# Kernel optimization log

Measured on AMD Instinct MI355X. Metric: run time of the kernel, lower is better.

## Reference

```python
import jax, jax.numpy as jnp
import numpy as np

N = 100000      # nodes
E = 1600000     # edges
IN = 64; H = 64; OUT = 64
ED = 32         # edge_dim
L = 2           # num_layers
NT = 3          # num_node_types
ET = 4          # num_edge_types
EPS = 1e-5


def setup_inputs() -> dict:
    key = jax.random.key(0)
    ks = jax.random.split(key, 16)
    x = jax.random.normal(ks[0], (N, IN), dtype=jnp.float32)
    edge_index = jax.random.randint(ks[1], (2, E), 0, N, dtype=jnp.int64)
    edge_attr = jax.random.normal(ks[2], (E, ED), dtype=jnp.float32)
    node_type = jax.random.randint(ks[3], (N,), 0, NT, dtype=jnp.int64)
    edge_type = jax.random.randint(ks[4], (E,), 0, ET, dtype=jnp.int64)
    # parameters (stacked over layers; layer0 in_channels == hidden so shapes match)
    Wn = jax.random.normal(ks[5], (L, NT, H, H), dtype=jnp.float32) * 0.05   # per-node-type linear
    bn = jax.random.normal(ks[6], (L, NT, H), dtype=jnp.float32) * 0.05
    Wm = jax.random.normal(ks[7], (L, ET, ED), dtype=jnp.float32) * 0.1     # edge MLP Linear(ED,1)
    bm = jax.random.normal(ks[8], (L, ET), dtype=jnp.float32) * 0.1
    emb = jax.random.normal(ks[9], (L, ET, ED), dtype=jnp.float32) * 0.1    # edge_type_emb
    ln_g = jnp.ones((L, H), dtype=jnp.float32)
    ln_b = jnp.zeros((L, H), dtype=jnp.float32)
    fc_w = jax.random.normal(ks[10], (OUT, H), dtype=jnp.float32) * 0.05
    fc_b = jnp.zeros((OUT,), dtype=jnp.float32)
    return {"x": x, "edge_index": edge_index, "edge_attr": edge_attr,
            "node_type": node_type, "edge_type": edge_type,
            "Wn": Wn, "bn": bn, "Wm": Wm, "bm": bm, "emb": emb,
            "ln_g": ln_g, "ln_b": ln_b, "fc_w": fc_w, "fc_b": fc_b}


def _layernorm(h, g, b):
    mu = jnp.mean(h, axis=-1, keepdims=True)
    var = jnp.mean((h - mu) ** 2, axis=-1, keepdims=True)
    return (h - mu) * jax.lax.rsqrt(var + EPS) * g + b


def reference(x, edge_index, edge_attr, node_type, edge_type,
              Wn, bn, Wm, bm, emb, ln_g, ln_b, fc_w, fc_b):
    src = edge_index[0]  # x_j
    dst = edge_index[1]  # x_i (aggregation target)
    for l in range(L):
        # HydroConv message: softplus(edge MLP per edge type) * (x_j - x_i)
        ea = edge_attr + emb[l][edge_type]                               # [E, ED]
        w = jax.nn.softplus(jnp.einsum('ed,ed->e', ea, Wm[l][edge_type])
                            + bm[l][edge_type])                          # [E]
        msg = w[:, None] * (x[src] - x[dst])                             # [E, H]
        aggr = jax.ops.segment_sum(msg, dst, num_segments=N)            # [N, H]
        # per-node-type linear update
        h = jnp.einsum('nd,ndo->no', aggr, Wn[l][node_type]) + bn[l][node_type]
        h = jax.nn.relu(h)
        x = _layernorm(h, ln_g[l], ln_b[l])
    return x @ fc_w.T + fc_b
```

## Files before the change

kernel.cpp:

```cpp
#include <hip/hip_runtime.h>

#define NN 100000
#define NE 1600000
#define HDIM 64
#define EDIM 32
#define NTT 3
#define ETT 4
#define NTILES 6250
#define LEPS 1e-5f
#define NBKT 782
#define EPB 8192
#define NWGA 196
#define SCAP 4096
#define NSC (NBKT * NWGA)
#define SBLK 150

typedef _Float16 half2v __attribute__((ext_vector_type(2)));
typedef _Float16 half4v __attribute__((ext_vector_type(4)));
typedef _Float16 half8v __attribute__((ext_vector_type(8)));
typedef float f32x4 __attribute__((ext_vector_type(4)));

__global__ void prep_kernel(const float* __restrict__ Wn, const float* __restrict__ fc_w,
                            _Float16* __restrict__ Wp, _Float16* __restrict__ fcp) {
    const int i = blockIdx.x * blockDim.x + threadIdx.x;
    if (i < 6 * HDIM * HDIM) {
        const int lt = i >> 12;
        const int o = (i >> 6) & 63;
        const int d = i & 63;
        Wp[i] = (_Float16)Wn[((size_t)lt * 64 + d) * 64 + o];
    } else if (i < 6 * HDIM * HDIM + HDIM * HDIM) {
        const int j = i - 6 * HDIM * HDIM;
        fcp[j] = (_Float16)fc_w[j];
    }
}

__global__ __launch_bounds__(256) void edge_weights_kernel(
        const float* __restrict__ edge_attr,
        const int* __restrict__ eisrc,
        const int* __restrict__ edge_type,
        const float* __restrict__ Wm,
        const float* __restrict__ bm,
        const float* __restrict__ emb,
        int2* __restrict__ ewu) {
    __shared__ float sWm[2 * ETT * EDIM];
    __shared__ float sc[2 * ETT];
    const int tid = threadIdx.x;
    if (tid < 2 * ETT * EDIM) sWm[tid] = Wm[tid];
    __syncthreads();
    if (tid < 2 * ETT) {
        float c = bm[tid];
        #pragma unroll
        for (int k = 0; k < EDIM; k++) c += emb[tid * EDIM + k] * sWm[tid * EDIM + k];
        sc[tid] = c;
    }
    __syncthreads();
    const int lane = tid & 63;
    const int wv = tid >> 6;
    const int sub = lane >> 3;
    const int k = lane & 7;
    const int ebase = blockIdx.x * 128 + wv * 32;
    #pragma unroll
    for (int it = 0; it < 4; it++) {
        const int e = ebase + it * 8 + sub;
        const int et = edge_type[e];
        const float4 v = ((const float4*)(edge_attr + (size_t)e * EDIM))[k];
        const float4 a = ((const float4*)(sWm + et * EDIM))[k];
        const float4 b = ((const float4*)(sWm + (ETT + et) * EDIM))[k];
        float d0 = v.x * a.x + v.y * a.y + v.z * a.z + v.w * a.w;
        float d1 = v.x * b.x + v.y * b.y + v.z * b.z + v.w * b.w;
        d0 += __shfl_xor(d0, 1); d1 += __shfl_xor(d1, 1);
        d0 += __shfl_xor(d0, 2); d1 += __shfl_xor(d1, 2);
        d0 += __shfl_xor(d0, 4); d1 += __shfl_xor(d1, 4);
        if (k == 0) {
            d0 += sc[et];
            d1 += sc[ETT + et];
            const float w0 = fmaxf(d0, 0.f) + log1pf(expf(-fabsf(d0)));
            const float w1 = fmaxf(d1, 0.f) + log1pf(expf(-fabsf(d1)));
            union { half2v h; int i; } u;
            u.h[0] = (_Float16)w0;
            u.h[1] = (_Float16)w1;
            ewu[e] = make_int2(u.i, eisrc[e]);
        }
    }
}

__global__ void xcvt_kernel(const float* __restrict__ x, _Float16* __restrict__ xs) {
    const int i = blockIdx.x * blockDim.x + threadIdx.x;
    const float4 v = ((const float4*)x)[i];
    half4v o = { (_Float16)v.x, (_Float16)v.y, (_Float16)v.z, (_Float16)v.w };
    ((half4v*)xs)[i] = o;
}

__global__ __launch_bounds__(256) void hist_kernel(const int* __restrict__ eidst,
                                                   int* __restrict__ whist) {
    __shared__ int h[NBKT];
    for (int i = threadIdx.x; i < NBKT; i += 256) h[i] = 0;
    __syncthreads();
    const int wg = blockIdx.x;
    const int start = wg * EPB, end = min(start + EPB, NE);
    for (int e = start + threadIdx.x; e < end; e += 256)
        atomicAdd(&h[eidst[e] >> 7], 1);
    __syncthreads();
    for (int i = threadIdx.x; i < NBKT; i += 256) whist[i * NWGA + wg] = h[i];
}

__global__ __launch_bounds__(256) void partial2_kernel(const int* __restrict__ in,
                                                       int* __restrict__ psum) {
    __shared__ int red[256];
    const int b = blockIdx.x, t = threadIdx.x;
    const int base = b * 1024 + t * 4;
    int s = 0;
    #pragma unroll
    for (int k = 0; k < 4; k++) { const int i = base + k; if (i < NSC) s += in[i]; }
    red[t] = s;
    __syncthreads();
    for (int d = 128; d > 0; d >>= 1) {
        if (t < d) red[t] += red[t + d];
        __syncthreads();
    }
    if (t == 0) psum[b] = red[0];
}

__global__ void bscan2_kernel(const int* __restrict__ psum, int* __restrict__ poff) {
    __shared__ int v[256];
    const int t = threadIdx.x;
    v[t] = (t < SBLK) ? psum[t] : 0;
    __syncthreads();
    for (int d = 1; d < 256; d <<= 1) {
        const int x = (t >= d) ? v[t - d] : 0;
        __syncthreads();
        v[t] += x;
        __syncthreads();
    }
    poff[t] = (t == 0) ? 0 : v[t - 1];
}

__global__ __launch_bounds__(256) void wscan2_kernel(const int* __restrict__ in,
                                                     const int* __restrict__ poff,
                                                     int* __restrict__ out) {
    __shared__ int red[256];
    const int b = blockIdx.x, t = threadIdx.x;
    const int base = b * 1024 + t * 4;
    int d4[4];
    #pragma unroll
    for (int k = 0; k < 4; k++) d4[k] = (base + k < NSC) ? in[base + k] : 0;
    const int s = d4[0] + d4[1] + d4[2] + d4[3];
    red[t] = s;
    __syncthreads();
    for (int d = 1; d < 256; d <<= 1) {
        const int x = (t >= d) ? red[t - d] : 0;
        __syncthreads();
        red[t] += x;
        __syncthreads();
    }
    int run = poff[b] + ((t == 0) ? 0 : red[t - 1]);
    #pragma unroll
    for (int k = 0; k < 4; k++) {
        if (base + k < NSC) { out[base + k] = run; run += d4[k]; }
    }
}

__global__ __launch_bounds__(256) void binb_kernel(const int2* __restrict__ ewu,
                                                   const int* __restrict__ eidst,
                                                   const int* __restrict__ wscan,
                                                   int2* __restrict__ brec) {
    __shared__ int lcur[NBKT];
    const int wg = blockIdx.x;
    for (int i = threadIdx.x; i < NBKT; i += 256) lcur[i] = wscan[i * NWGA + wg];
    __syncthreads();
    const int start = wg * EPB, end = min(start + EPB, NE);
    for (int e = start + threadIdx.x; e < end; e += 256) {
        const int dst = eidst[e];
        const int2 r = ewu[e];
        const int pos = atomicAdd(&lcur[dst >> 7], 1);
        brec[pos] = make_int2(r.x, r.y | ((dst & 127) << 17));
    }
}

__global__ __launch_bounds__(256) void sortb_kernel(const int2* __restrict__ brec,
                                                    const int* __restrict__ wscan,
                                                    int* __restrict__ off,
                                                    int2* __restrict__ ews) {
    __shared__ int hist[128];
    __shared__ int excl[128];
    __shared__ int2 sorted[SCAP];
    const int b = blockIdx.x;
    const int node0 = b << 7;
    const int nn = min(128, NN - node0);
    const int base = wscan[b * NWGA];
    const int end = (b < NBKT - 1) ? wscan[(b + 1) * NWGA] : NE;
    const int n = end - base;
    const int t = threadIdx.x;
    if (t < 128) hist[t] = 0;
    __syncthreads();
    for (int i = t; i < n; i += 256)
        atomicAdd(&hist[(brec[base + i].y >> 17) & 127], 1);
    __syncthreads();
    if (t < 128) excl[t] = hist[t];
    __syncthreads();
    for (int d = 1; d < 128; d <<= 1) {
        int v = 0;
        if (t < 128 && t >= d) v = excl[t - d];
        __syncthreads();
        if (t < 128) excl[t] += v;
        __syncthreads();
    }
    if (t < 128) {
        const int ex = excl[t] - hist[t];
        if (t < nn) off[node0 + t] = base + ex;
        hist[t] = ex;
    }
    if (b == NBKT - 1 && t == 0) off[NN] = NE;
    __syncthreads();
    for (int i = t; i < n; i += 256) {
        const int2 r = brec[base + i];
        const int dstl = (r.y >> 17) & 127;
        const int2 o = make_int2(r.x, r.y & 0x1FFFF);
        const int pos = atomicAdd(&hist[dstl], 1);
        if (pos < SCAP) sorted[pos] = o;
        else ews[base + pos] = o;
    }
    __syncthreads();
    const int m = min(n, SCAP);
    for (int i = t; i < m; i += 256) ews[base + i] = sorted[i];
}

template<int LAYER>
__global__ __launch_bounds__(512) void gather_kernel(const _Float16* __restrict__ xs,
                                                     const int2* __restrict__ ew,
                                                     const int* __restrict__ off,
                                                     _Float16* __restrict__ aggr) {
    const int lane = threadIdx.x & 63;
    const int wid = threadIdx.x >> 6;
    const int p = blockIdx.x * 8 + wid;
    const int g = lane >> 4;
    const int fl = lane & 15;
    const int lo = off[p], hi = off[p + 1];
    float a0 = 0.f, a1 = 0.f, a2 = 0.f, a3 = 0.f, sw = 0.f;
    for (int base = lo; base < hi; base += 4) {
        const int i = base + g;
        if (i < hi) {
            const int2 e = ew[i];
            union { int i; half2v h; } u; u.i = e.x;
            const float w = (float)u.h[LAYER];
            const half4v xv = *(const half4v*)(xs + (size_t)e.y * HDIM + fl * 4);
            a0 += w * (float)xv[0];
            a1 += w * (float)xv[1];
            a2 += w * (float)xv[2];
            a3 += w * (float)xv[3];
            sw += w;
        }
    }
    a0 += __shfl_xor(a0, 16); a1 += __shfl_xor(a1, 16);
    a2 += __shfl_xor(a2, 16); a3 += __shfl_xor(a3, 16);
    sw += __shfl_xor(sw, 16);
    a0 += __shfl_xor(a0, 32); a1 += __shfl_xor(a1, 32);
    a2 += __shfl_xor(a2, 32); a3 += __shfl_xor(a3, 32);
    sw += __shfl_xor(sw, 32);
    const half4v xt = *(const half4v*)(xs + (size_t)p * HDIM + fl * 4);
    a0 -= sw * (float)xt[0];
    a1 -= sw * (float)xt[1];
    a2 -= sw * (float)xt[2];
    a3 -= sw * (float)xt[3];
    if (g == 0) {
        half4v o = { (_Float16)a0, (_Float16)a1, (_Float16)a2, (_Float16)a3 };
        *(half4v*)(aggr + (size_t)p * HDIM + fl * 4) = o;
    }
}

template<int FUSE>
__global__ __launch_bounds__(256) void update_kernel(const _Float16* __restrict__ aggr,
                                                     const int* __restrict__ ntype,
                                                     const _Float16* __restrict__ Wp,
                                                     const float* __restrict__ bnp,
                                                     const float* __restrict__ lng,
                                                     const float* __restrict__ lnb,
                                                     const _Float16* __restrict__ fcp,
                                                     const float* __restrict__ fcb,
                                                     _Float16* __restrict__ xout,
                                                     float* __restrict__ fout) {
    __shared__ float scst[320];
    __shared__ f32x4 sraw[4 * 4608 / 16];
    for (int i = threadIdx.x; i < 320; i += 256)
        scst[i] = (i < 192) ? bnp[i] : ((i < 256) ? lng[i - 192] : lnb[i - 256]);
    __syncthreads();

    const int wid = threadIdx.x >> 6;
    const int lane = threadIdx.x & 63;
    const int tile = blockIdx.x * 4 + wid;
    if (tile >= NTILES) return;
    const int fl = lane & 15;
    const int gq = lane >> 4;
    const size_t R = (size_t)tile * 16;

    const half8v A0 = *(const half8v*)(aggr + (R + fl) * HDIM + gq * 8);
    const half8v A1 = *(const half8v*)(aggr + (R + fl) * HDIM + 32 + gq * 8);
    int nt[4];
    #pragma unroll
    for (int r = 0; r < 4; r++) nt[r] = ntype[R + gq * 4 + r];

    float h[4][4];
    #pragma unroll
    for (int ob = 0; ob < 4; ob++) {
        const int col = ob * 16 + fl;
        f32x4 c[3];
        #pragma unroll
        for (int t = 0; t < 3; t++) {
            const half8v B0 = *(const half8v*)(Wp + t * 4096 + col * 64 + gq * 8);
            const half8v B1 = *(const half8v*)(Wp + t * 4096 + col * 64 + 32 + gq * 8);
            f32x4 z = { 0.f, 0.f, 0.f, 0.f };
            z = __builtin_amdgcn_mfma_f32_16x16x32_f16(A0, B0, z, 0, 0, 0);
            z = __builtin_amdgcn_mfma_f32_16x16x32_f16(A1, B1, z, 0, 0, 0);
            c[t] = z;
        }
        #pragma unroll
        for (int r = 0; r < 4; r++) {
            float v = (nt[r] == 0) ? c[0][r] : ((nt[r] == 1) ? c[1][r] : c[2][r]);
            v += scst[nt[r] * 64 + col];
            h[ob][r] = fmaxf(v, 0.f);
        }
    }

    float mu[4], rs[4];
    #pragma unroll
    for (int r = 0; r < 4; r++) {
        float m = h[0][r] + h[1][r] + h[2][r] + h[3][r];
        m += __shfl_xor(m, 1); m += __shfl_xor(m, 2);
        m += __shfl_xor(m, 4); m += __shfl_xor(m, 8);
        mu[r] = m * (1.f / 64.f);
        const float d0 = h[0][r] - mu[r], d1 = h[1][r] - mu[r];
        const float d2 = h[2][r] - mu[r], d3 = h[3][r] - mu[r];
        float v = d0 * d0 + d1 * d1 + d2 * d2 + d3 * d3;
        v += __shfl_xor(v, 1); v += __shfl_xor(v, 2);
        v += __shfl_xor(v, 4); v += __shfl_xor(v, 8);
        rs[r] = rsqrtf(v * (1.f / 64.f) + LEPS);
    }

    _Float16* wb = (_Float16*)sraw + (size_t)wid * 2304;
    #pragma unroll
    for (int ob = 0; ob < 4; ob++) {
        const int col = ob * 16 + fl;
        const float gg = scst[192 + col], bb = scst[256 + col];
        #pragma unroll
        for (int r = 0; r < 4; r++) {
            const float xn = (h[ob][r] - mu[r]) * rs[r] * gg + bb;
            wb[(gq * 4 + r) * 72 + col] = (_Float16)xn;
        }
    }
    __threadfence_block();

    if (!FUSE) {
        const int rr = lane >> 2, cg = lane & 3;
        const half8v o0 = *(const half8v*)(wb + rr * 72 + cg * 16);
        const half8v o1 = *(const half8v*)(wb + rr * 72 + cg * 16 + 8);
        *(half8v*)(xout + (R + rr) * HDIM + cg * 16) = o0;
        *(half8v*)(xout + (R + rr) * HDIM + cg * 16 + 8) = o1;
    } else {
        const half8v FA0 = *(const half8v*)(wb + fl * 72 + gq * 8);
        const half8v FA1 = *(const half8v*)(wb + fl * 72 + 32 + gq * 8);
        float fo[4][4];
        #pragma unroll
        for (int ob = 0; ob < 4; ob++) {
            const int col = ob * 16 + fl;
            const half8v FB0 = *(const half8v*)(fcp + col * 64 + gq * 8);
            const half8v FB1 = *(const half8v*)(fcp + col * 64 + 32 + gq * 8);
            f32x4 z = { 0.f, 0.f, 0.f, 0.f };
            z = __builtin_amdgcn_mfma_f32_16x16x32_f16(FA0, FB0, z, 0, 0, 0);
            z = __builtin_amdgcn_mfma_f32_16x16x32_f16(FA1, FB1, z, 0, 0, 0);
            const float fb = fcb[col];
            #pragma unroll
            for (int r = 0; r < 4; r++) fo[ob][r] = z[r] + fb;
        }
        __threadfence_block();
        float* fb32 = (float*)((char*)sraw + (size_t)wid * 4608);
        #pragma unroll
        for (int ob = 0; ob < 4; ob++) {
            const int col = ob * 16 + fl;
            #pragma unroll
            for (int r = 0; r < 4; r++) fb32[(gq * 4 + r) * 68 + col] = fo[ob][r];
        }
        __threadfence_block();
        #pragma unroll
        for (int rr = 0; rr < 16; rr++)
            fout[(R + rr) * HDIM + lane] = fb32[rr * 68 + lane];
    }
}

extern "C" void kernel_launch(void* const* d_in, const int* in_sizes, int n_in,
                              void* d_out, int out_size, void* d_ws, size_t ws_size,
                              hipStream_t stream) {
    const float* x         = (const float*)d_in[0];
    const int*   ei        = (const int*)d_in[1];
    const float* edge_attr = (const float*)d_in[2];
    const int*   node_type = (const int*)d_in[3];
    const int*   edge_type = (const int*)d_in[4];
    const float* Wn        = (const float*)d_in[5];
    const float* bn        = (const float*)d_in[6];
    const float* Wm        = (const float*)d_in[7];
    const float* bm        = (const float*)d_in[8];
    const float* emb       = (const float*)d_in[9];
    const float* ln_g      = (const float*)d_in[10];
    const float* ln_b      = (const float*)d_in[11];
    const float* fc_w      = (const float*)d_in[12];
    const float* fc_b      = (const float*)d_in[13];
    float* out = (float*)d_out;

    char* W = (char*)d_ws;
    int2*      ewu  = (int2*)W;
    int2*      ews  = (int2*)(W + 12800000);
    _Float16*  xs   = (_Float16*)(W + 25600000);
    _Float16*  x1s  = (_Float16*)(W + 38400000);
    _Float16*  aggr = (_Float16*)(W + 51200000);
    int2*      brec = (int2*)(W + 64000000);
    char*      p3   = W + 76800000;
    _Float16*  Wp   = (_Float16*)p3;
    _Float16*  fcp  = (_Float16*)(p3 + 49152);
    int*       off  = (int*)(p3 + 49152 + 8192);
    int*       psum2 = off + NN + 16;
    int*       poff2 = psum2 + 256;
    int*       whist = poff2 + 256;
    int*       wscan = whist + NSC;

    prep_kernel<<<112, 256, 0, stream>>>(Wn, fc_w, Wp, fcp);
    edge_weights_kernel<<<NE / 128, 256, 0, stream>>>(edge_attr, ei, edge_type,
                                                      Wm, bm, emb, ewu);
    xcvt_kernel<<<6250, 256, 0, stream>>>(x, xs);

    hist_kernel<<<NWGA, 256, 0, stream>>>(ei + NE, whist);
    partial2_kernel<<<SBLK, 256, 0, stream>>>(whist, psum2);
    bscan2_kernel<<<1, 256, 0, stream>>>(psum2, poff2);
    wscan2_kernel<<<SBLK, 256, 0, stream>>>(whist, poff2, wscan);
    binb_kernel<<<NWGA, 256, 0, stream>>>(ewu, ei + NE, wscan, brec);
    sortb_kernel<<<NBKT, 256, 0, stream>>>(brec, wscan, off, ews);

    gather_kernel<0><<<NN / 8, 512, 0, stream>>>(xs, ews, off, aggr);
    update_kernel<0><<<(NTILES + 3) / 4, 256, 0, stream>>>(aggr, node_type,
        Wp, bn, ln_g, ln_b, fcp, fc_b, x1s, nullptr);
    gather_kernel<1><<<NN / 8, 512, 0, stream>>>(x1s, ews, off, aggr);
    update_kernel<1><<<(NTILES + 3) / 4, 256, 0, stream>>>(aggr, node_type,
        Wp + 3 * 4096, bn + NTT * HDIM, ln_g + HDIM, ln_b + HDIM, fcp, fc_b, nullptr, out);
}
```

Measured before the change: 332.8 us.

## Fuse gather and per-type update into one layer kernel via shared memory

```diff
diff --git a/kernel.cpp b/kernel.cpp
--- a/kernel.cpp
+++ b/kernel.cpp
@@ -225,76 +225,83 @@
     for (int i = t; i < m; i += 256) ews[base + i] = sorted[i];
 }
 
-template<int LAYER>
-__global__ __launch_bounds__(512) void gather_kernel(const _Float16* __restrict__ xs,
-                                                     const int2* __restrict__ ew,
-                                                     const int* __restrict__ off,
-                                                     _Float16* __restrict__ aggr) {
-    const int lane = threadIdx.x & 63;
-    const int wid = threadIdx.x >> 6;
-    const int p = blockIdx.x * 8 + wid;
-    const int g = lane >> 4;
-    const int fl = lane & 15;
-    const int lo = off[p], hi = off[p + 1];
-    float a0 = 0.f, a1 = 0.f, a2 = 0.f, a3 = 0.f, sw = 0.f;
-    for (int base = lo; base < hi; base += 4) {
-        const int i = base + g;
-        if (i < hi) {
-            const int2 e = ew[i];
-            union { int i; half2v h; } u; u.i = e.x;
-            const float w = (float)u.h[LAYER];
-            const half4v xv = *(const half4v*)(xs + (size_t)e.y * HDIM + fl * 4);
-            a0 += w * (float)xv[0];
-            a1 += w * (float)xv[1];
-            a2 += w * (float)xv[2];
-            a3 += w * (float)xv[3];
-            sw += w;
-        }
-    }
-    a0 += __shfl_xor(a0, 16); a1 += __shfl_xor(a1, 16);
-    a2 += __shfl_xor(a2, 16); a3 += __shfl_xor(a3, 16);
-    sw += __shfl_xor(sw, 16);
-    a0 += __shfl_xor(a0, 32); a1 += __shfl_xor(a1, 32);
-    a2 += __shfl_xor(a2, 32); a3 += __shfl_xor(a3, 32);
-    sw += __shfl_xor(sw, 32);
-    const half4v xt = *(const half4v*)(xs + (size_t)p * HDIM + fl * 4);
-    a0 -= sw * (float)xt[0];
-    a1 -= sw * (float)xt[1];
-    a2 -= sw * (float)xt[2];
-    a3 -= sw * (float)xt[3];
-    if (g == 0) {
-        half4v o = { (_Float16)a0, (_Float16)a1, (_Float16)a2, (_Float16)a3 };
-        *(half4v*)(aggr + (size_t)p * HDIM + fl * 4) = o;
-    }
-}
-
-template<int FUSE>
-__global__ __launch_bounds__(256) void update_kernel(const _Float16* __restrict__ aggr,
-                                                     const int* __restrict__ ntype,
-                                                     const _Float16* __restrict__ Wp,
-                                                     const float* __restrict__ bnp,
-                                                     const float* __restrict__ lng,
-                                                     const float* __restrict__ lnb,
-                                                     const _Float16* __restrict__ fcp,
-                                                     const float* __restrict__ fcb,
-                                                     _Float16* __restrict__ xout,
-                                                     float* __restrict__ fout) {
+template<int LAYER, int FUSE>
+__global__ __launch_bounds__(512) void layer_kernel(
+        const _Float16* __restrict__ xs,
+        const int2* __restrict__ ew,
+        const int* __restrict__ off,
+        const int* __restrict__ ntype,
+        const _Float16* __restrict__ Wp,
+        const float* __restrict__ bnp,
+        const float* __restrict__ lng,
+        const float* __restrict__ lnb,
+        const _Float16* __restrict__ fcp,
+        const float* __restrict__ fcb,
+        _Float16* __restrict__ xout,
+        float* __restrict__ fout) {
     __shared__ float scst[320];
-    __shared__ f32x4 sraw[4 * 4608 / 16];
-    for (int i = threadIdx.x; i < 320; i += 256)
+    __shared__ _Float16 wb[16 * 72];
+    __shared__ float fb32[16 * 68];
+    const int tid = threadIdx.x;
+    for (int i = tid; i < 320; i += 512)
         scst[i] = (i < 192) ? bnp[i] : ((i < 256) ? lng[i - 192] : lnb[i - 256]);
-    __syncthreads();
-
-    const int wid = threadIdx.x >> 6;
-    const int lane = threadIdx.x & 63;
-    const int tile = blockIdx.x * 4 + wid;
-    if (tile >= NTILES) return;
+
+    const int wv = tid >> 6;
+    const int lane = tid & 63;
+    const int sub = lane >> 3;
+    const int k = lane & 7;
+    const size_t R = (size_t)blockIdx.x * 16;
+
+    #pragma unroll
+    for (int rep = 0; rep < 2; rep++) {
+        const int nl = wv * 2 + rep;
+        const int p = (int)R + nl;
+        const int lo = off[p], hi = off[p + 1];
+        float a0 = 0.f, a1 = 0.f, a2 = 0.f, a3 = 0.f;
+        float a4 = 0.f, a5 = 0.f, a6 = 0.f, a7 = 0.f, sw = 0.f;
+        for (int base = lo; base < hi; base += 8) {
+            const int i = base + sub;
+            if (i < hi) {
+                const int2 e = ew[i];
+                union { int i; half2v h; } u; u.i = e.x;
+                const float w = (float)u.h[LAYER];
+                const half8v xv = *(const half8v*)(xs + (size_t)e.y * HDIM + k * 8);
+                a0 += w * (float)xv[0]; a1 += w * (float)xv[1];
+                a2 += w * (float)xv[2]; a3 += w * (float)xv[3];
+                a4 += w * (float)xv[4]; a5 += w * (float)xv[5];
+                a6 += w * (float)xv[6]; a7 += w * (float)xv[7];
+                sw += w;
+            }
+        }
+        #pragma unroll
+        for (int d = 8; d < 64; d <<= 1) {
+            a0 += __shfl_xor(a0, d); a1 += __shfl_xor(a1, d);
+            a2 += __shfl_xor(a2, d); a3 += __shfl_xor(a3, d);
+            a4 += __shfl_xor(a4, d); a5 += __shfl_xor(a5, d);
+            a6 += __shfl_xor(a6, d); a7 += __shfl_xor(a7, d);
+            sw += __shfl_xor(sw, d);
+        }
+        if (sub == 0) {
+            const half8v xt = *(const half8v*)(xs + (size_t)((int)R + nl) * HDIM + k * 8);
+            half8v o;
+            o[0] = (_Float16)(a0 - sw * (float)xt[0]);
+            o[1] = (_Float16)(a1 - sw * (float)xt[1]);
+            o[2] = (_Float16)(a2 - sw * (float)xt[2]);
+            o[3] = (_Float16)(a3 - sw * (float)xt[3]);
+            o[4] = (_Float16)(a4 - sw * (float)xt[4]);
+            o[5] = (_Float16)(a5 - sw * (float)xt[5]);
+            o[6] = (_Float16)(a6 - sw * (float)xt[6]);
+            o[7] = (_Float16)(a7 - sw * (float)xt[7]);
+            *(half8v*)(&wb[nl * 72 + k * 8]) = o;
+        }
+    }
+    __syncthreads();
+    if (wv != 0) return;
+
     const int fl = lane & 15;
     const int gq = lane >> 4;
-    const size_t R = (size_t)tile * 16;
-
-    const half8v A0 = *(const half8v*)(aggr + (R + fl) * HDIM + gq * 8);
-    const half8v A1 = *(const half8v*)(aggr + (R + fl) * HDIM + 32 + gq * 8);
+    const half8v A0 = *(const half8v*)(&wb[fl * 72 + gq * 8]);
+    const half8v A1 = *(const half8v*)(&wb[fl * 72 + 32 + gq * 8]);
     int nt[4];
     #pragma unroll
     for (int r = 0; r < 4; r++) nt[r] = ntype[R + gq * 4 + r];
@@ -336,7 +343,6 @@
         rs[r] = rsqrtf(v * (1.f / 64.f) + LEPS);
     }
 
-    _Float16* wb = (_Float16*)sraw + (size_t)wid * 2304;
     #pragma unroll
     for (int ob = 0; ob < 4; ob++) {
         const int col = ob * 16 + fl;
@@ -351,13 +357,13 @@
 
     if (!FUSE) {
         const int rr = lane >> 2, cg = lane & 3;
-        const half8v o0 = *(const half8v*)(wb + rr * 72 + cg * 16);
-        const half8v o1 = *(const half8v*)(wb + rr * 72 + cg * 16 + 8);
+        const half8v o0 = *(const half8v*)(&wb[rr * 72 + cg * 16]);
+        const half8v o1 = *(const half8v*)(&wb[rr * 72 + cg * 16 + 8]);
         *(half8v*)(xout + (R + rr) * HDIM + cg * 16) = o0;
         *(half8v*)(xout + (R + rr) * HDIM + cg * 16 + 8) = o1;
     } else {
-        const half8v FA0 = *(const half8v*)(wb + fl * 72 + gq * 8);
-        const half8v FA1 = *(const half8v*)(wb + fl * 72 + 32 + gq * 8);
+        const half8v FA0 = *(const half8v*)(&wb[fl * 72 + gq * 8]);
+        const half8v FA1 = *(const half8v*)(&wb[fl * 72 + 32 + gq * 8]);
         float fo[4][4];
         #pragma unroll
         for (int ob = 0; ob < 4; ob++) {
@@ -371,8 +377,6 @@
             #pragma unroll
             for (int r = 0; r < 4; r++) fo[ob][r] = z[r] + fb;
         }
-        __threadfence_block();
-        float* fb32 = (float*)((char*)sraw + (size_t)wid * 4608);
         #pragma unroll
         for (int ob = 0; ob < 4; ob++) {
             const int col = ob * 16 + fl;
@@ -410,9 +414,8 @@
     int2*      ews  = (int2*)(W + 12800000);
     _Float16*  xs   = (_Float16*)(W + 25600000);
     _Float16*  x1s  = (_Float16*)(W + 38400000);
-    _Float16*  aggr = (_Float16*)(W + 51200000);
-    int2*      brec = (int2*)(W + 64000000);
-    char*      p3   = W + 76800000;
+    int2*      brec = (int2*)(W + 51200000);
+    char*      p3   = W + 64000000;
     _Float16*  Wp   = (_Float16*)p3;
     _Float16*  fcp  = (_Float16*)(p3 + 49152);
     int*       off  = (int*)(p3 + 49152 + 8192);
@@ -433,10 +436,9 @@
     binb_kernel<<<NWGA, 256, 0, stream>>>(ewu, ei + NE, wscan, brec);
     sortb_kernel<<<NBKT, 256, 0, stream>>>(brec, wscan, off, ews);
 
-    gather_kernel<0><<<NN / 8, 512, 0, stream>>>(xs, ews, off, aggr);
-    update_kernel<0><<<(NTILES + 3) / 4, 256, 0, stream>>>(aggr, node_type,
+    layer_kernel<0, 0><<<NTILES, 512, 0, stream>>>(xs, ews, off, node_type,
         Wp, bn, ln_g, ln_b, fcp, fc_b, x1s, nullptr);
-    gather_kernel<1><<<NN / 8, 512, 0, stream>>>(x1s, ews, off, aggr);
-    update_kernel<1><<<(NTILES + 3) / 4, 256, 0, stream>>>(aggr, node_type,
-        Wp + 3 * 4096, bn + NTT * HDIM, ln_g + HDIM, ln_b + HDIM, fcp, fc_b, nullptr, out);
-}
+    layer_kernel<1, 1><<<NTILES, 512, 0, stream>>>(x1s, ews, off, node_type,
+        Wp + 3 * 4096, bn + NTT * HDIM, ln_g + HDIM, ln_b + HDIM, fcp, fc_b,
+        nullptr, out);
+}
```

After: 340.4 us. +2.3%, slower.
